# Performance work log

Measured on AMD Instinct MI355X. Metric: run time of the kernel, lower is better.

## Reference

```python
import jax, jax.numpy as jnp
import numpy as np

B, S, K, D = 512, 64, 8, 16
NE, NR, NU = 2_000_000, 64, 10_000
NSTEPS, NUNITS, NITER = 100, 128, 2


def _alpha_schedule():
    # betas = sigmoid(linspace(-6,6)) * (0.005 - 1e-5) + 1e-5; alphas_prod = cumprod(1-betas)
    betas = jax.nn.sigmoid(jnp.linspace(-6.0, 6.0, NSTEPS)) * (0.005 - 1e-5) + 1e-5
    aprod = jnp.cumprod(1.0 - betas)
    return jnp.sqrt(aprod), jnp.sqrt(1.0 - aprod)


def _forward(usr_emb, ent_emb, rel_emb, agg_W, agg_b, fc1_W, fc1_b, fc2_W, fc2_b,
             mlp_W1, mlp_b1, mlp_W2, mlp_b2, mlp_W3, mlp_b3, mlp_W4, mlp_b4,
             step_emb1, step_emb2, step_emb3, noise_e, u, v, click_seq, adj_ent, adj_rel, t):
    user = usr_emb[u]                                   # [B,D]
    # --- diffusion branch: x = x0*sqrt(abar_t) + e*sqrt(1-abar_t), then MLP with step-emb adds
    abar_sqrt, ombar_sqrt = _alpha_schedule()
    x = user * abar_sqrt[t][:, None] + noise_e * ombar_sqrt[t][:, None]
    for Wl, bl, se in ((mlp_W1, mlp_b1, step_emb1), (mlp_W2, mlp_b2, step_emb2), (mlp_W3, mlp_b3, step_emb3)):
        x = jax.nn.relu(x @ Wl + bl + se[t])            # [B,128]
    diff_out = x @ mlp_W4 + mlp_b4                      # [B,D]
    # --- multi-hop neighbor gather (entities/relations per hop)
    e0 = click_seq                                      # [B,S]
    e1 = adj_ent[e0]                                    # [B,S,K]
    e2 = adj_ent[e1].reshape(B, S, K * K)               # [B,S,K*K]
    r0 = adj_rel[e0]                                    # [B,S,K]
    r1 = adj_rel[e1].reshape(B, S, K * K)               # [B,S,K*K]
    ev = [ent_emb[e0][:, :, None, :], ent_emb[e1], ent_emb[e2]]  # [B,S,1,D],[B,S,K,D],[B,S,K*K,D]
    rv = [rel_emb[r0], rel_emb[r1]]

    def aggregate(self_v, neigh_v, rel_v, act):
        # KGCN sum-aggregator: user-relation score softmax over neighbors, weighted sum, linear, act
        scores = jnp.mean(user[:, None, None, None, :] * rel_v, axis=-1)   # [B,S,n,K]
        p = jax.nn.softmax(scores, axis=-1)
        neigh_agg = jnp.einsum('bsnk,bsnkd->bsnd', p, neigh_v)             # [B,S,n,D]
        return act((self_v + neigh_agg) @ agg_W + agg_b)

    for i in range(NITER):
        act = jnp.tanh if i == NITER - 1 else jax.nn.sigmoid
        nxt = []
        for hop in range(NITER - i):
            n_self = ev[hop].shape[2]
            nv = ev[hop + 1].reshape(B, S, n_self, K, D)
            relv = rv[hop].reshape(B, S, n_self, K, D)
            nxt.append(aggregate(ev[hop], nv, relv, act))
        ev = nxt
    item_emb = jax.nn.relu(ev[0].reshape(B, S, D))      # relu applied twice in source == once
    trans = item_emb                                    # Transform treated as identity (code unavailable)
    s_sum = jax.nn.relu(jnp.sum(trans, axis=1))         # [B,D]
    s_max = jax.nn.relu(jnp.max(trans, axis=1))         # [B,D]
    fusion = jnp.concatenate([s_sum, s_max], axis=1)    # [B,2D]
    feat = jax.nn.relu(jax.nn.relu(fusion @ fc1_W + fc1_b) @ fc2_W + fc2_b)  # [B,D]
    outs = jax.nn.sigmoid(jnp.sum(feat * ent_emb[v], axis=1))               # [B]
    return jnp.concatenate([outs[:, None], diff_out], axis=1)               # [B,1+D]


def setup_inputs() -> dict:
    key = jax.random.key(0)
    ks = iter(jax.random.split(key, 32))
    nrm = lambda shape, s: jax.random.normal(next(ks), shape, dtype=jnp.float32) * s
    zf = lambda shape: jnp.zeros(shape, dtype=jnp.float32)
    ri = lambda shape, hi: jax.random.randint(next(ks), shape, 0, hi, dtype=jnp.int32)
    return {
        'usr_emb': nrm((NU, D), 0.1), 'ent_emb': nrm((NE, D), 0.1), 'rel_emb': nrm((NR, D), 0.1),
        'agg_W': nrm((D, D), 0.25), 'agg_b': zf((D,)),
        'fc1_W': nrm((2 * D, 64), 0.18), 'fc1_b': zf((64,)),
        'fc2_W': nrm((64, D), 0.125), 'fc2_b': zf((D,)),
        'mlp_W1': nrm((D, NUNITS), 0.25), 'mlp_b1': zf((NUNITS,)),
        'mlp_W2': nrm((NUNITS, NUNITS), 0.09), 'mlp_b2': zf((NUNITS,)),
        'mlp_W3': nrm((NUNITS, NUNITS), 0.09), 'mlp_b3': zf((NUNITS,)),
        'mlp_W4': nrm((NUNITS, D), 0.09), 'mlp_b4': zf((D,)),
        'step_emb1': nrm((NSTEPS, NUNITS), 0.1), 'step_emb2': nrm((NSTEPS, NUNITS), 0.1),
        'step_emb3': nrm((NSTEPS, NUNITS), 0.1),
        'noise_e': jax.random.normal(next(ks), (B, D), dtype=jnp.float32),
        'u': ri((B,), NU), 'v': ri((B,), NE), 'click_seq': ri((B, S), NE),
        'adj_ent': ri((NE, K), NE), 'adj_rel': ri((NE, K), NR), 't': ri((B,), NSTEPS),
    }


def reference(usr_emb, ent_emb, rel_emb, agg_W, agg_b, fc1_W, fc1_b, fc2_W, fc2_b,
              mlp_W1, mlp_b1, mlp_W2, mlp_b2, mlp_W3, mlp_b3, mlp_W4, mlp_b4,
              step_emb1, step_emb2, step_emb3, noise_e, u, v, click_seq, adj_ent, adj_rel, t):
    return _forward(usr_emb, ent_emb, rel_emb, agg_W, agg_b, fc1_W, fc1_b, fc2_W, fc2_b,
                    mlp_W1, mlp_b1, mlp_W2, mlp_b2, mlp_W3, mlp_b3, mlp_W4, mlp_b4,
                    step_emb1, step_emb2, step_emb3, noise_e, u, v, click_seq, adj_ent, adj_rel, t)
```

## Files before the change

### kernel.cpp

```cpp
#include <hip/hip_runtime.h>
#include <math.h>

namespace {
constexpr int B = 512, S = 64, K = 8, D = 16, NR = 64, NSTEPS = 100, NUNITS = 128;
}

#define WAVE_LDS_FENCE() __asm__ volatile("s_waitcnt lgkmcnt(0)" ::: "memory")

__global__ __launch_bounds__(256) void k_prep_all(
    const float* __restrict__ usr_emb, const float* __restrict__ rel_emb,
    const int* __restrict__ u, const int* __restrict__ click_seq,
    const int* __restrict__ adj_ent, const int* __restrict__ adj_rel,
    float* __restrict__ w_tab, int* __restrict__ e1s, int* __restrict__ r0s,
    float* __restrict__ sa, float* __restrict__ so)
{
    int b = blockIdx.x, t = threadIdx.x;
    if (t < 64) {
        const float* ur = usr_emb + (long)u[b] * D;
        const float* rr = rel_emb + t * D;
        float s = 0.f;
#pragma unroll
        for (int d = 0; d < D; ++d) s += ur[d] * rr[d];
        w_tab[b * NR + t] = s * (1.0f / 16.0f);
    } else if (t < 128) {
        int p = b * S + (t - 64);
        int e0 = click_seq[p];
        const int4* ae = (const int4*)(adj_ent + (long)e0 * K);
        const int4* ar = (const int4*)(adj_rel + (long)e0 * K);
        int4 a0 = ae[0], a1 = ae[1], b0 = ar[0], b1 = ar[1];
        int4* oe = (int4*)(e1s + (long)p * K);
        int4* orr = (int4*)(r0s + (long)p * K);
        oe[0] = a0; oe[1] = a1;
        orr[0] = b0; orr[1] = b1;
    } else if (b == 0 && (t - 128) < NSTEPS) {
        int i = t - 128;
        float prod = 1.0f;
        for (int jj = 0; jj <= i; ++jj) {
            float x = -6.0f + (float)jj * (12.0f / 99.0f);
            float sig = 1.0f / (1.0f + expf(-x));
            prod *= (1.0f - (sig * (0.005f - 1e-5f) + 1e-5f));
        }
        sa[i] = sqrtf(prod);
        so[i] = sqrtf(1.0f - prod);
    }
}

__global__ __launch_bounds__(256) void k_kgcn(
    const float* __restrict__ ent_emb,
    const float* __restrict__ w_tab,
    const int* __restrict__ click_seq,
    const int* __restrict__ adj_ent,
    const int* __restrict__ adj_rel,
    const int* __restrict__ e1s,
    const int* __restrict__ r0s,
    const float* __restrict__ agg_W,
    const float* __restrict__ agg_b,
    float* __restrict__ item)
{
    __shared__ float wb[4][NR];
    __shared__ float Ws[4][D][D + 1];
    __shared__ float bs[4][D];
    __shared__ float Ms[4][K][D + 1];
    __shared__ float h1s[4][K][D + 1];
    __shared__ float h0s[4][D];
    __shared__ float A0s[4][D];
    __shared__ float M1s[4][D];
    __shared__ float p0s[4][K];

    const int tid = threadIdx.x;
    const int w = tid >> 6;
    const int lane = tid & 63;
    const int p = blockIdx.x * 4 + w;
    const int b = p >> 6;
    const int k = lane >> 3, j = lane & 7;

    const int e0 = click_seq[p];
    const int e1k = e1s[(long)p * K + k];
    const int r0k = r0s[(long)p * K + k];
    const int e2kj = adj_ent[(long)e1k * K + j];
    const int r1kj = adj_rel[(long)e1k * K + j];

    {
        const float4 wv = ((const float4*)agg_W)[lane];
        int row = lane >> 2, col = (lane & 3) * 4;
        Ws[w][row][col] = wv.x; Ws[w][row][col + 1] = wv.y;
        Ws[w][row][col + 2] = wv.z; Ws[w][row][col + 3] = wv.w;
        wb[w][lane] = w_tab[b * NR + lane];
        if (lane < D) bs[w][lane] = agg_b[lane];
    }
    WAVE_LDS_FENCE();

    float s1 = wb[w][r1kj];
    float m1 = s1;
    m1 = fmaxf(m1, __shfl_xor(m1, 1));
    m1 = fmaxf(m1, __shfl_xor(m1, 2));
    m1 = fmaxf(m1, __shfl_xor(m1, 4));
    float ex = expf(s1 - m1);
    float den = ex;
    den += __shfl_xor(den, 1);
    den += __shfl_xor(den, 2);
    den += __shfl_xor(den, 4);
    float p1 = ex / den;

    float q2r[D], q1r[D], q0r[D];
    {
        const float4* q2p = (const float4*)(ent_emb + (long)e2kj * D);
        float4 a0 = q2p[0], a1 = q2p[1], a2 = q2p[2], a3 = q2p[3];
        q2r[0]=a0.x; q2r[1]=a0.y; q2r[2]=a0.z; q2r[3]=a0.w;
        q2r[4]=a1.x; q2r[5]=a1.y; q2r[6]=a1.z; q2r[7]=a1.w;
        q2r[8]=a2.x; q2r[9]=a2.y; q2r[10]=a2.z; q2r[11]=a2.w;
        q2r[12]=a3.x; q2r[13]=a3.y; q2r[14]=a3.z; q2r[15]=a3.w;
    }
    {
        const float4* q1p = (const float4*)(ent_emb + (long)e1k * D);
        float4 a0 = q1p[0], a1 = q1p[1], a2 = q1p[2], a3 = q1p[3];
        q1r[0]=a0.x; q1r[1]=a0.y; q1r[2]=a0.z; q1r[3]=a0.w;
        q1r[4]=a1.x; q1r[5]=a1.y; q1r[6]=a1.z; q1r[7]=a1.w;
        q1r[8]=a2.x; q1r[9]=a2.y; q1r[10]=a2.z; q1r[11]=a2.w;
        q1r[12]=a3.x; q1r[13]=a3.y; q1r[14]=a3.z; q1r[15]=a3.w;
    }
    {
        const float4* q0p = (const float4*)(ent_emb + (long)e0 * D);
        float4 a0 = q0p[0], a1 = q0p[1], a2 = q0p[2], a3 = q0p[3];
        q0r[0]=a0.x; q0r[1]=a0.y; q0r[2]=a0.z; q0r[3]=a0.w;
        q0r[4]=a1.x; q0r[5]=a1.y; q0r[6]=a1.z; q0r[7]=a1.w;
        q0r[8]=a2.x; q0r[9]=a2.y; q0r[10]=a2.z; q0r[11]=a2.w;
        q0r[12]=a3.x; q0r[13]=a3.y; q0r[14]=a3.z; q0r[15]=a3.w;
    }

    {
        float cur[16];
#pragma unroll
        for (int d = 0; d < 16; ++d) cur[d] = p1 * q2r[d];
        const bool b0 = (lane & 1), b1 = (lane & 2), b2 = (lane & 4);
        float n8[8];
#pragma unroll
        for (int d = 0; d < 8; ++d) {
            float snd = b0 ? cur[d] : cur[d + 8];
            float kp  = b0 ? cur[d + 8] : cur[d];
            n8[d] = kp + __shfl_xor(snd, 1);
        }
        float n4[4];
#pragma unroll
        for (int d = 0; d < 4; ++d) {
            float snd = b1 ? n8[d] : n8[d + 4];
            float kp  = b1 ? n8[d + 4] : n8[d];
            n4[d] = kp + __shfl_xor(snd, 2);
        }
        float a0 = (b2 ? n4[2] : n4[0]) + __shfl_xor(b2 ? n4[0] : n4[2], 4);
        float a1 = (b2 ? n4[3] : n4[1]) + __shfl_xor(b2 ? n4[1] : n4[3], 4);
        const int dbase = (b0 ? 8 : 0) + (b1 ? 4 : 0) + (b2 ? 2 : 0);
        Ms[w][k][dbase]     = q1r[dbase]     + a0;
        Ms[w][k][dbase + 1] = q1r[dbase + 1] + a1;
    }

    float s0 = wb[w][r0k];
    float m0 = s0;
    m0 = fmaxf(m0, __shfl_xor(m0, 8));
    m0 = fmaxf(m0, __shfl_xor(m0, 16));
    m0 = fmaxf(m0, __shfl_xor(m0, 32));
    float e0x = expf(s0 - m0);
    float d0 = e0x;
    d0 += __shfl_xor(d0, 8);
    d0 += __shfl_xor(d0, 16);
    d0 += __shfl_xor(d0, 32);
    float p0 = e0x / d0;
    if (j == 0) p0s[w][k] = p0;

    {
        float cur[16];
#pragma unroll
        for (int d = 0; d < 16; ++d) cur[d] = p0 * q1r[d];
        const bool c0 = (lane & 8), c1 = (lane & 16), c2 = (lane & 32);
        float n8[8];
#pragma unroll
        for (int d = 0; d < 8; ++d) {
            float snd = c0 ? cur[d] : cur[d + 8];
            float kp  = c0 ? cur[d + 8] : cur[d];
            n8[d] = kp + __shfl_xor(snd, 8);
        }
        float n4[4];
#pragma unroll
        for (int d = 0; d < 4; ++d) {
            float snd = c1 ? n8[d] : n8[d + 4];
            float kp  = c1 ? n8[d + 4] : n8[d];
            n4[d] = kp + __shfl_xor(snd, 16);
        }
        float a0 = (c2 ? n4[2] : n4[0]) + __shfl_xor(c2 ? n4[0] : n4[2], 32);
        float a1 = (c2 ? n4[3] : n4[1]) + __shfl_xor(c2 ? n4[1] : n4[3], 32);
        const int dbase = (c0 ? 8 : 0) + (c1 ? 4 : 0) + (c2 ? 2 : 0);
        if (j == 0) { A0s[w][dbase] = a0; A0s[w][dbase + 1] = a1; }
    }
    WAVE_LDS_FENCE();

#pragma unroll
    for (int o = lane; o < 128; o += 64) {
        int ko = o >> 4, dd = o & 15;
        float acc = bs[w][dd];
#pragma unroll
        for (int din = 0; din < D; ++din) acc += Ms[w][ko][din] * Ws[w][din][dd];
        h1s[w][ko][dd] = 1.0f / (1.0f + expf(-acc));
    }

    const int ddl = lane & 15;
    {
        float acc = bs[w][ddl];
#pragma unroll
        for (int din = 0; din < D; ++din)
            acc += (q0r[din] + A0s[w][din]) * Ws[w][din][ddl];
        if (lane < D) h0s[w][lane] = 1.0f / (1.0f + expf(-acc));
    }
    WAVE_LDS_FENCE();

    if (lane < D) {
        float m = h0s[w][lane];
#pragma unroll
        for (int kk = 0; kk < K; ++kk) m += p0s[w][kk] * h1s[w][kk][lane];
        M1s[w][lane] = m;
    }
    WAVE_LDS_FENCE();

    {
        float acc = bs[w][ddl];
#pragma unroll
        for (int din = 0; din < D; ++din) acc += M1s[w][din] * Ws[w][din][ddl];
        if (lane < D) item[(long)p * D + lane] = fmaxf(tanhf(acc), 0.0f);
    }
}

__global__ __launch_bounds__(128) void k_tail(
    const float* __restrict__ item,
    const float* __restrict__ fc1_W, const float* __restrict__ fc1_b,
    const float* __restrict__ fc2_W, const float* __restrict__ fc2_b,
    const float* __restrict__ ent_emb, const int* __restrict__ v,
    const float* __restrict__ usr_emb, const float* __restrict__ noise_e,
    const int* __restrict__ u, const int* __restrict__ t_arr,
    const float* __restrict__ W1, const float* __restrict__ b1,
    const float* __restrict__ W2, const float* __restrict__ b2,
    const float* __restrict__ W3, const float* __restrict__ b3,
    const float* __restrict__ W4, const float* __restrict__ b4,
    const float* __restrict__ se1, const float* __restrict__ se2,
    const float* __restrict__ se3,
    const float* __restrict__ sa, const float* __restrict__ so,
    float* __restrict__ out)
{
    __shared__ float x0[D];
    __shared__ float ha[NUNITS];
    __shared__ float hb[NUNITS];
    __shared__ float sm[S][D + 1];
    __shared__ float fus[2 * D];
    __shared__ float hid[64];
    __shared__ float feat_s[D];

    int b = blockIdx.x, t = threadIdx.x;
    int ts = t_arr[b];

    if (t < D)
        x0[t] = usr_emb[(long)u[b] * D + t] * sa[ts] + noise_e[(long)b * D + t] * so[ts];
    __syncthreads();

    float a = b1[t] + se1[(long)ts * NUNITS + t];
#pragma unroll
    for (int i = 0; i < D; ++i) a += x0[i] * W1[i * NUNITS + t];
    ha[t] = fmaxf(a, 0.0f);
    __syncthreads();

    a = b2[t] + se2[(long)ts * NUNITS + t];
    for (int i = 0; i < NUNITS; ++i) a += ha[i] * W2[i * NUNITS + t];
    hb[t] = fmaxf(a, 0.0f);
    __syncthreads();

    a = b3[t] + se3[(long)ts * NUNITS + t];
    for (int i = 0; i < NUNITS; ++i) a += hb[i] * W3[i * NUNITS + t];
    __syncthreads();
    ha[t] = fmaxf(a, 0.0f);
    __syncthreads();

    if (t < D) {
        float acc = b4[t];
        for (int i = 0; i < NUNITS; ++i) acc += ha[i] * W4[i * D + t];
        out[(long)b * 17 + 1 + t] = acc;
    }

    if (t < 64) {
        const float4* ip = (const float4*)(item + ((long)b * S + t) * D);
        float4 r0 = ip[0], r1 = ip[1], r2 = ip[2], r3 = ip[3];
        sm[t][0]=r0.x;  sm[t][1]=r0.y;  sm[t][2]=r0.z;  sm[t][3]=r0.w;
        sm[t][4]=r1.x;  sm[t][5]=r1.y;  sm[t][6]=r1.z;  sm[t][7]=r1.w;
        sm[t][8]=r2.x;  sm[t][9]=r2.y;  sm[t][10]=r2.z; sm[t][11]=r2.w;
        sm[t][12]=r3.x; sm[t][13]=r3.y; sm[t][14]=r3.z; sm[t][15]=r3.w;
    }
    __syncthreads();

    if (t < D) {
        float sv = 0.0f, mv = -1e30f;
        for (int ss = 0; ss < S; ++ss) {
            float x = sm[ss][t];
            sv += x;
            mv = fmaxf(mv, x);
        }
        fus[t] = fmaxf(sv, 0.0f);
        fus[D + t] = fmaxf(mv, 0.0f);
    }
    __syncthreads();

    if (t < 64) {
        float acc = fc1_b[t];
#pragma unroll
        for (int i = 0; i < 2 * D; ++i) acc += fus[i] * fc1_W[i * 64 + t];
        hid[t] = fmaxf(acc, 0.0f);
    }
    __syncthreads();

    if (t < D) {
        float f = fc2_b[t];
#pragma unroll
        for (int i = 0; i < 64; ++i) f += hid[i] * fc2_W[i * D + t];
        feat_s[t] = fmaxf(f, 0.0f);
    }
    __syncthreads();

    if (t < D) {
        float g = feat_s[t] * ent_emb[(long)v[b] * D + t];
        g += __shfl_xor(g, 1);
        g += __shfl_xor(g, 2);
        g += __shfl_xor(g, 4);
        g += __shfl_xor(g, 8);
        if (t == 0) out[(long)b * 17] = 1.0f / (1.0f + expf(-g));
    }
}

extern "C" void kernel_launch(void* const* d_in, const int* in_sizes, int n_in,
                              void* d_out, int out_size, void* d_ws, size_t ws_size,
                              hipStream_t stream) {
    const float* usr_emb = (const float*)d_in[0];
    const float* ent_emb = (const float*)d_in[1];
    const float* rel_emb = (const float*)d_in[2];
    const float* agg_W   = (const float*)d_in[3];
    const float* agg_b   = (const float*)d_in[4];
    const float* fc1_W   = (const float*)d_in[5];
    const float* fc1_b   = (const float*)d_in[6];
    const float* fc2_W   = (const float*)d_in[7];
    const float* fc2_b   = (const float*)d_in[8];
    const float* mlp_W1  = (const float*)d_in[9];
    const float* mlp_b1  = (const float*)d_in[10];
    const float* mlp_W2  = (const float*)d_in[11];
    const float* mlp_b2  = (const float*)d_in[12];
    const float* mlp_W3  = (const float*)d_in[13];
    const float* mlp_b3  = (const float*)d_in[14];
    const float* mlp_W4  = (const float*)d_in[15];
    const float* mlp_b4  = (const float*)d_in[16];
    const float* se1     = (const float*)d_in[17];
    const float* se2     = (const float*)d_in[18];
    const float* se3     = (const float*)d_in[19];
    const float* noise_e = (const float*)d_in[20];
    const int* u         = (const int*)d_in[21];
    const int* v         = (const int*)d_in[22];
    const int* click_seq = (const int*)d_in[23];
    const int* adj_ent   = (const int*)d_in[24];
    const int* adj_rel   = (const int*)d_in[25];
    const int* t         = (const int*)d_in[26];
    float* out = (float*)d_out;

    float* ws = (float*)d_ws;
    float* w_tab = ws;
    float* sa    = w_tab + B * NR;
    float* so    = sa + 128;
    float* item  = so + 128;
    int*   e1s   = (int*)(item + B * S * D);
    int*   r0s   = e1s + B * S * K;

    k_prep_all<<<B, 256, 0, stream>>>(usr_emb, rel_emb, u, click_seq, adj_ent, adj_rel,
                                      w_tab, e1s, r0s, sa, so);
    k_kgcn<<<(B * S) / 4, 256, 0, stream>>>(ent_emb, w_tab, click_seq, adj_ent, adj_rel,
                                            e1s, r0s, agg_W, agg_b, item);
    k_tail<<<B, 128, 0, stream>>>(item, fc1_W, fc1_b, fc2_W, fc2_b, ent_emb, v,
                                  usr_emb, noise_e, u, t, mlp_W1, mlp_b1, mlp_W2, mlp_b2,
                                  mlp_W3, mlp_b3, mlp_W4, mlp_b4, se1, se2, se3, sa, so, out);
}
```

Before: 335.7 us.

## Stage gathered entity rows in swizzled LDS with coalesced float4 loads

The KGCN kernel now writes all 73 entity indices per position into LDS and has the wave cooperatively gather the embedding rows into a swizzled LDS row buffer, instead of each lane loading three full 16-float rows into registers. Cross-lane reductions then read from LDS instead of running butterfly shuffle trees, and the relation-score table and intermediate results move from LDS into registers and are exchanged with shuffles. This is meant to cut redundant global gathers (q1/q0 rows were loaded by many lanes) and register pressure, at the cost of more LDS traffic and a larger LDS footprint per block.

```diff
diff --git a/kernel.cpp b/kernel.cpp
--- a/kernel.cpp
+++ b/kernel.cpp
@@ -3,9 +3,12 @@
 
 namespace {
 constexpr int B = 512, S = 64, K = 8, D = 16, NR = 64, NSTEPS = 100, NUNITS = 128;
+constexpr int NROWS = 73;
 }
 
 #define WAVE_LDS_FENCE() __asm__ volatile("s_waitcnt lgkmcnt(0)" ::: "memory")
+
+__device__ __forceinline__ int rowoff(int r) { return r * 16 + ((r >> 3) & 7) * 4; }
 
 __global__ __launch_bounds__(256) void k_prep_all(
     const float* __restrict__ usr_emb, const float* __restrict__ rel_emb,
@@ -57,15 +60,10 @@
     const float* __restrict__ agg_b,
     float* __restrict__ item)
 {
-    __shared__ float wb[4][NR];
-    __shared__ float Ws[4][D][D + 1];
-    __shared__ float bs[4][D];
-    __shared__ float Ms[4][K][D + 1];
-    __shared__ float h1s[4][K][D + 1];
-    __shared__ float h0s[4][D];
-    __shared__ float A0s[4][D];
-    __shared__ float M1s[4][D];
-    __shared__ float p0s[4][K];
+    __shared__ int   idxs[4][80];
+    __shared__ float rowbuf[4][1184];
+    __shared__ float Ws[4][D][17];
+    __shared__ float Ms[4][K][18];
 
     const int tid = threadIdx.x;
     const int w = tid >> 6;
@@ -74,158 +72,111 @@
     const int b = p >> 6;
     const int k = lane >> 3, j = lane & 7;
 
-    const int e0 = click_seq[p];
-    const int e1k = e1s[(long)p * K + k];
-    const int r0k = r0s[(long)p * K + k];
+    const int e0   = click_seq[p];
+    const int e1k  = e1s[(long)p * K + k];
+    const int r0k  = r0s[(long)p * K + k];
     const int e2kj = adj_ent[(long)e1k * K + j];
     const int r1kj = adj_rel[(long)e1k * K + j];
-
+    const float wv   = w_tab[b * NR + lane];
+    const float bval = agg_b[lane & 15];
     {
-        const float4 wv = ((const float4*)agg_W)[lane];
+        const float4 wq = ((const float4*)agg_W)[lane];
         int row = lane >> 2, col = (lane & 3) * 4;
-        Ws[w][row][col] = wv.x; Ws[w][row][col + 1] = wv.y;
-        Ws[w][row][col + 2] = wv.z; Ws[w][row][col + 3] = wv.w;
-        wb[w][lane] = w_tab[b * NR + lane];
-        if (lane < D) bs[w][lane] = agg_b[lane];
-    }
+        Ws[w][row][col] = wq.x; Ws[w][row][col + 1] = wq.y;
+        Ws[w][row][col + 2] = wq.z; Ws[w][row][col + 3] = wq.w;
+    }
+    idxs[w][lane] = e2kj;
+    if (j == 0) idxs[w][64 + k] = e1k;
+    if (lane == 0) idxs[w][72] = e0;
     WAVE_LDS_FENCE();
 
-    float s1 = wb[w][r1kj];
+    float s1 = __shfl(wv, r1kj);
     float m1 = s1;
     m1 = fmaxf(m1, __shfl_xor(m1, 1));
     m1 = fmaxf(m1, __shfl_xor(m1, 2));
     m1 = fmaxf(m1, __shfl_xor(m1, 4));
     float ex = expf(s1 - m1);
     float den = ex;
-    den += __shfl_xor(den, 1);
-    den += __shfl_xor(den, 2);
-    den += __shfl_xor(den, 4);
-    float p1 = ex / den;
-
-    float q2r[D], q1r[D], q0r[D];
-    {
-        const float4* q2p = (const float4*)(ent_emb + (long)e2kj * D);
-        float4 a0 = q2p[0], a1 = q2p[1], a2 = q2p[2], a3 = q2p[3];
-        q2r[0]=a0.x; q2r[1]=a0.y; q2r[2]=a0.z; q2r[3]=a0.w;
-        q2r[4]=a1.x; q2r[5]=a1.y; q2r[6]=a1.z; q2r[7]=a1.w;
-        q2r[8]=a2.x; q2r[9]=a2.y; q2r[10]=a2.z; q2r[11]=a2.w;
-        q2r[12]=a3.x; q2r[13]=a3.y; q2r[14]=a3.z; q2r[15]=a3.w;
-    }
-    {
-        const float4* q1p = (const float4*)(ent_emb + (long)e1k * D);
-        float4 a0 = q1p[0], a1 = q1p[1], a2 = q1p[2], a3 = q1p[3];
-        q1r[0]=a0.x; q1r[1]=a0.y; q1r[2]=a0.z; q1r[3]=a0.w;
-        q1r[4]=a1.x; q1r[5]=a1.y; q1r[6]=a1.z; q1r[7]=a1.w;
-        q1r[8]=a2.x; q1r[9]=a2.y; q1r[10]=a2.z; q1r[11]=a2.w;
-        q1r[12]=a3.x; q1r[13]=a3.y; q1r[14]=a3.z; q1r[15]=a3.w;
-    }
-    {
-        const float4* q0p = (const float4*)(ent_emb + (long)e0 * D);
-        float4 a0 = q0p[0], a1 = q0p[1], a2 = q0p[2], a3 = q0p[3];
-        q0r[0]=a0.x; q0r[1]=a0.y; q0r[2]=a0.z; q0r[3]=a0.w;
-        q0r[4]=a1.x; q0r[5]=a1.y; q0r[6]=a1.z; q0r[7]=a1.w;
-        q0r[8]=a2.x; q0r[9]=a2.y; q0r[10]=a2.z; q0r[11]=a2.w;
-        q0r[12]=a3.x; q0r[13]=a3.y; q0r[14]=a3.z; q0r[15]=a3.w;
-    }
-
-    {
-        float cur[16];
-#pragma unroll
-        for (int d = 0; d < 16; ++d) cur[d] = p1 * q2r[d];
-        const bool b0 = (lane & 1), b1 = (lane & 2), b2 = (lane & 4);
-        float n8[8];
-#pragma unroll
-        for (int d = 0; d < 8; ++d) {
-            float snd = b0 ? cur[d] : cur[d + 8];
-            float kp  = b0 ? cur[d + 8] : cur[d];
-            n8[d] = kp + __shfl_xor(snd, 1);
-        }
-        float n4[4];
-#pragma unroll
-        for (int d = 0; d < 4; ++d) {
-            float snd = b1 ? n8[d] : n8[d + 4];
-            float kp  = b1 ? n8[d + 4] : n8[d];
-            n4[d] = kp + __shfl_xor(snd, 2);
-        }
-        float a0 = (b2 ? n4[2] : n4[0]) + __shfl_xor(b2 ? n4[0] : n4[2], 4);
-        float a1 = (b2 ? n4[3] : n4[1]) + __shfl_xor(b2 ? n4[1] : n4[3], 4);
-        const int dbase = (b0 ? 8 : 0) + (b1 ? 4 : 0) + (b2 ? 2 : 0);
-        Ms[w][k][dbase]     = q1r[dbase]     + a0;
-        Ms[w][k][dbase + 1] = q1r[dbase + 1] + a1;
-    }
-
-    float s0 = wb[w][r0k];
+    den += __shfl_xor(den, 1); den += __shfl_xor(den, 2); den += __shfl_xor(den, 4);
+    const float p1 = ex / den;
+
+    float s0 = __shfl(wv, r0k);
     float m0 = s0;
     m0 = fmaxf(m0, __shfl_xor(m0, 8));
     m0 = fmaxf(m0, __shfl_xor(m0, 16));
     m0 = fmaxf(m0, __shfl_xor(m0, 32));
     float e0x = expf(s0 - m0);
     float d0 = e0x;
-    d0 += __shfl_xor(d0, 8);
-    d0 += __shfl_xor(d0, 16);
-    d0 += __shfl_xor(d0, 32);
-    float p0 = e0x / d0;
-    if (j == 0) p0s[w][k] = p0;
-
+    d0 += __shfl_xor(d0, 8); d0 += __shfl_xor(d0, 16); d0 += __shfl_xor(d0, 32);
+    const float p0 = e0x / d0;
+
+#pragma unroll
+    for (int it = 0; it < 5; ++it) {
+        int t = it * 64 + lane;
+        if (t < NROWS * 4) {
+            int r = t >> 2, seg = t & 3;
+            const float4 v = *(const float4*)(ent_emb + (long)idxs[w][r] * D + seg * 4);
+            *(float4*)&rowbuf[w][rowoff(r) + seg * 4] = v;
+        }
+    }
+    WAVE_LDS_FENCE();
+
+    const int h = j;
+    float acc0 = 0.f, acc1 = 0.f;
+#pragma unroll
+    for (int jp = 0; jp < 8; ++jp) {
+        float pw = __shfl(p1, k * 8 + jp);
+        const float2 q = *(const float2*)&rowbuf[w][rowoff(k * 8 + jp) + 2 * h];
+        acc0 += pw * q.x;
+        acc1 += pw * q.y;
+    }
     {
-        float cur[16];
-#pragma unroll
-        for (int d = 0; d < 16; ++d) cur[d] = p0 * q1r[d];
-        const bool c0 = (lane & 8), c1 = (lane & 16), c2 = (lane & 32);
-        float n8[8];
-#pragma unroll
-        for (int d = 0; d < 8; ++d) {
-            float snd = c0 ? cur[d] : cur[d + 8];
-            float kp  = c0 ? cur[d + 8] : cur[d];
-            n8[d] = kp + __shfl_xor(snd, 8);
+        const float2 q1v = *(const float2*)&rowbuf[w][rowoff(64 + k) + 2 * h];
+        Ms[w][k][2 * h]     = q1v.x + acc0;
+        Ms[w][k][2 * h + 1] = q1v.y + acc1;
+    }
+
+    const int kq = lane >> 4, dl = lane & 15;
+    const float p0a = __shfl(p0, kq * 8);
+    const float p0b = __shfl(p0, (kq + 4) * 8);
+    float ag = p0a * rowbuf[w][rowoff(64 + kq) + dl]
+             + p0b * rowbuf[w][rowoff(64 + kq + 4) + dl];
+    ag += __shfl_xor(ag, 16);
+    ag += __shfl_xor(ag, 32);
+    WAVE_LDS_FENCE();
+
+    float h1a, h1b;
+    {
+        float a1 = bval, a2 = bval;
+#pragma unroll
+        for (int din = 0; din < D; ++din) {
+            float wcol = Ws[w][din][dl];
+            a1 += Ms[w][kq][din]     * wcol;
+            a2 += Ms[w][kq + 4][din] * wcol;
         }
-        float n4[4];
-#pragma unroll
-        for (int d = 0; d < 4; ++d) {
-            float snd = c1 ? n8[d] : n8[d + 4];
-            float kp  = c1 ? n8[d + 4] : n8[d];
-            n4[d] = kp + __shfl_xor(snd, 16);
-        }
-        float a0 = (c2 ? n4[2] : n4[0]) + __shfl_xor(c2 ? n4[0] : n4[2], 32);
-        float a1 = (c2 ? n4[3] : n4[1]) + __shfl_xor(c2 ? n4[1] : n4[3], 32);
-        const int dbase = (c0 ? 8 : 0) + (c1 ? 4 : 0) + (c2 ? 2 : 0);
-        if (j == 0) { A0s[w][dbase] = a0; A0s[w][dbase + 1] = a1; }
-    }
-    WAVE_LDS_FENCE();
-
-#pragma unroll
-    for (int o = lane; o < 128; o += 64) {
-        int ko = o >> 4, dd = o & 15;
-        float acc = bs[w][dd];
-#pragma unroll
-        for (int din = 0; din < D; ++din) acc += Ms[w][ko][din] * Ws[w][din][dd];
-        h1s[w][ko][dd] = 1.0f / (1.0f + expf(-acc));
-    }
-
-    const int ddl = lane & 15;
-    {
-        float acc = bs[w][ddl];
-#pragma unroll
-        for (int din = 0; din < D; ++din)
-            acc += (q0r[din] + A0s[w][din]) * Ws[w][din][ddl];
-        if (lane < D) h0s[w][lane] = 1.0f / (1.0f + expf(-acc));
-    }
-    WAVE_LDS_FENCE();
-
-    if (lane < D) {
-        float m = h0s[w][lane];
-#pragma unroll
-        for (int kk = 0; kk < K; ++kk) m += p0s[w][kk] * h1s[w][kk][lane];
-        M1s[w][lane] = m;
-    }
-    WAVE_LDS_FENCE();
-
-    {
-        float acc = bs[w][ddl];
-#pragma unroll
-        for (int din = 0; din < D; ++din) acc += M1s[w][din] * Ws[w][din][ddl];
-        if (lane < D) item[(long)p * D + lane] = fmaxf(tanhf(acc), 0.0f);
-    }
+        h1a = 1.0f / (1.0f + expf(-a1));
+        h1b = 1.0f / (1.0f + expf(-a2));
+    }
+
+    float a0acc = bval;
+#pragma unroll
+    for (int din = 0; din < D; ++din) {
+        float q0d = rowbuf[w][rowoff(72) + din];
+        float agd = __shfl(ag, din);
+        a0acc += (q0d + agd) * Ws[w][din][dl];
+    }
+    const float h0v = 1.0f / (1.0f + expf(-a0acc));
+
+    float v1 = p0a * h1a + p0b * h1b;
+    v1 += __shfl_xor(v1, 16);
+    v1 += __shfl_xor(v1, 32);
+    const float M1 = h0v + v1;
+
+    float fin = bval;
+#pragma unroll
+    for (int din = 0; din < D; ++din)
+        fin += __shfl(M1, din) * Ws[w][din][dl];
+    if (lane < D) item[(long)p * D + lane] = fmaxf(tanhf(fin), 0.0f);
 }
 
 __global__ __launch_bounds__(128) void k_tail(
```

Result: no change. 338.0 us (+0.7%).
